# Optimization experiments

Hardware: AMD Instinct MI355X
Metric: run time of the kernel (lower is better)

The kernel has to match this reference:

```python
import jax, jax.numpy as jnp
import numpy as np


def setup_inputs() -> dict:
    key = jax.random.key(0)
    ks = jax.random.split(key, 6)
    B, T, I, H, O = 64, 512, 256, 512, 256
    stdv = 1.0 / np.sqrt(H)
    u = lambda k, shape: jax.random.uniform(k, shape, jnp.float32, -stdv, stdv)
    return {
        "x": jax.random.normal(ks[0], (B, T, I), jnp.float32),
        "W": u(ks[1], (I, 4 * H)),
        "U": u(ks[2], (H, 4 * H)),
        "bias": u(ks[3], (4 * H,)),
        "Wl": u(ks[4], (H, O)),
        "bl": u(ks[5], (O,)),
    }


def lstm_scan(x, W, U, bias):
    B, T, I = x.shape
    H = U.shape[0]
    # Precompute input projections for all timesteps in one big GEMM: [B,T,4H]
    x_proj = jnp.einsum("bti,ig->btg", x, W) + bias

    def step(carry, xp_t):
        h, c = carry
        gates = xp_t + h @ U  # [B, 4H]
        i_t = jax.nn.sigmoid(gates[:, :H])
        f_t = jax.nn.sigmoid(gates[:, H:2 * H])
        g_t = jnp.tanh(gates[:, 2 * H:3 * H])
        o_t = jax.nn.sigmoid(gates[:, 3 * H:])
        c_new = f_t * c + i_t * g_t
        h_new = o_t * jnp.tanh(c_new)
        return (h_new, c_new), h_new

    h0 = jnp.zeros((B, H), x.dtype)
    c0 = jnp.zeros((B, H), x.dtype)
    (h_T, c_T), hs = jax.lax.scan(step, (h0, c0), jnp.swapaxes(x_proj, 0, 1))
    hidden_seq = jnp.swapaxes(hs, 0, 1)  # [B, T, H]
    return hidden_seq, h_T, c_T


def reference(x, W, U, bias, Wl, bl):
    hidden_seq, h_T, c_T = lstm_scan(x, W, U, bias)
    out = hidden_seq @ Wl + bl  # [B, T, O]
    return out, (h_T, c_T)
```

## Files before the change

kernel.cpp:

```cpp
#include <hip/hip_runtime.h>
#include <stdint.h>

typedef uint16_t u16;
typedef uint32_t u32;
typedef unsigned long long u64;
typedef __attribute__((ext_vector_type(8))) __bf16 bf16x8;
typedef __attribute__((ext_vector_type(8))) short short8;
typedef __attribute__((ext_vector_type(4))) float floatx4;

__device__ __forceinline__ float bf2f(u16 u) {
  union { u32 i; float f; } v; v.i = ((u32)u) << 16; return v.f;
}
__device__ __forceinline__ u16 f2bf(float f) {
  union { float f; u32 i; } v; v.f = f;
  u32 i = v.i;
  return (u16)((i + 0x7FFFu + ((i >> 16) & 1u)) >> 16);
}
__device__ __forceinline__ float sigm(float x) { return 1.f / (1.f + __expf(-x)); }
__device__ __forceinline__ float tanh_f(float x) {
  x = fminf(15.f, fmaxf(-15.f, x));
  float e = __expf(2.f * x);
  return (e - 1.f) / (e + 1.f);
}

__global__ void transpose_f32_bf16(const float* __restrict__ src, u16* __restrict__ dst,
                                   int R, int C) {
  __shared__ u16 tile[32][33];
  int x = blockIdx.x * 32 + threadIdx.x;
#pragma unroll
  for (int j = 0; j < 4; ++j) {
    int y = blockIdx.y * 32 + threadIdx.y + j * 8;
    if (x < C && y < R) tile[threadIdx.y + j * 8][threadIdx.x] = f2bf(src[(size_t)y * C + x]);
  }
  __syncthreads();
  int x2 = blockIdx.y * 32 + threadIdx.x;
#pragma unroll
  for (int j = 0; j < 4; ++j) {
    int y2 = blockIdx.x * 32 + threadIdx.y + j * 8;
    if (x2 < R && y2 < C) dst[(size_t)y2 * R + x2] = tile[threadIdx.x][threadIdx.y + j * 8];
  }
}

__global__ __launch_bounds__(256) void gemm_a32_bt(
    const float* __restrict__ A, const u16* __restrict__ BT,
    const float* __restrict__ bias, u16* __restrict__ C,
    int M, int N, int K) {
  __shared__ __align__(16) u16 As[64 * 40];
  __shared__ __align__(16) u16 Bs[64 * 40];
  const int tid = threadIdx.x;
  const int wave = tid >> 6, lane = tid & 63;
  const int q4 = lane >> 4, n16 = lane & 15;
  const int mw = (wave >> 1) * 32, nw = (wave & 1) * 32;
  const int m0 = blockIdx.y * 64, n0 = blockIdx.x * 64;
  const int ldrow = tid >> 2, ldseg = (tid & 3) * 8;

  floatx4 acc[2][2] = {};
  for (int k0 = 0; k0 < K; k0 += 32) {
    const float* ap = A + (size_t)(m0 + ldrow) * K + k0 + ldseg;
    floatx4 a0 = *(const floatx4*)ap;
    floatx4 a1 = *(const floatx4*)(ap + 4);
    short8 s;
    s[0] = (short)f2bf(a0[0]); s[1] = (short)f2bf(a0[1]);
    s[2] = (short)f2bf(a0[2]); s[3] = (short)f2bf(a0[3]);
    s[4] = (short)f2bf(a1[0]); s[5] = (short)f2bf(a1[1]);
    s[6] = (short)f2bf(a1[2]); s[7] = (short)f2bf(a1[3]);
    *(short8*)(As + ldrow * 40 + ldseg) = s;
    *(short8*)(Bs + ldrow * 40 + ldseg) =
        *(const short8*)(BT + (size_t)(n0 + ldrow) * K + k0 + ldseg);
    __syncthreads();
#pragma unroll
    for (int mi = 0; mi < 2; ++mi) {
      bf16x8 a = *(const bf16x8*)(As + (mw + mi * 16 + n16) * 40 + q4 * 8);
#pragma unroll
      for (int ni = 0; ni < 2; ++ni) {
        bf16x8 b = *(const bf16x8*)(Bs + (nw + ni * 16 + n16) * 40 + q4 * 8);
        acc[mi][ni] = __builtin_amdgcn_mfma_f32_16x16x32_bf16(a, b, acc[mi][ni], 0, 0, 0);
      }
    }
    __syncthreads();
  }
#pragma unroll
  for (int mi = 0; mi < 2; ++mi)
#pragma unroll
    for (int ni = 0; ni < 2; ++ni) {
      int col = n0 + nw + ni * 16 + n16;
      float bv = bias[col];
#pragma unroll
      for (int r = 0; r < 4; ++r) {
        int m = m0 + mw + mi * 16 + q4 * 4 + r;
        C[(size_t)m * N + col] = f2bf(acc[mi][ni][r] + bv);
      }
    }
}

__global__ __launch_bounds__(256) void gemm_bt_f32out_perm(
    const u16* __restrict__ A, const u16* __restrict__ BT,
    const float* __restrict__ bias, float* __restrict__ C,
    int M, int N, int K) {
  __shared__ __align__(16) u16 As[64 * 40];
  __shared__ __align__(16) u16 Bs[64 * 40];
  const int tid = threadIdx.x;
  const int wave = tid >> 6, lane = tid & 63;
  const int q4 = lane >> 4, n16 = lane & 15;
  const int mw = (wave >> 1) * 32, nw = (wave & 1) * 32;
  const int m0 = blockIdx.y * 64, n0 = blockIdx.x * 64;
  const int ldrow = tid >> 2, ldseg = (tid & 3) * 8;

  const int mm = m0 + ldrow;
  const size_t slot = ((size_t)((mm >> 13) * 512 + ((mm & 8191) >> 4))) * 8192
                      + (mm & 15) * 16;

  floatx4 acc[2][2] = {};
  for (int k0 = 0; k0 < K; k0 += 32) {
    int kk = k0 + ldseg;
    *(short8*)(As + ldrow * 40 + ldseg) =
        *(const short8*)(A + slot + (kk >> 4) * 256 + (kk & 15));
    *(short8*)(Bs + ldrow * 40 + ldseg) =
        *(const short8*)(BT + (size_t)(n0 + ldrow) * K + k0 + ldseg);
    __syncthreads();
#pragma unroll
    for (int mi = 0; mi < 2; ++mi) {
      bf16x8 a = *(const bf16x8*)(As + (mw + mi * 16 + n16) * 40 + q4 * 8);
#pragma unroll
      for (int ni = 0; ni < 2; ++ni) {
        bf16x8 b = *(const bf16x8*)(Bs + (nw + ni * 16 + n16) * 40 + q4 * 8);
        acc[mi][ni] = __builtin_amdgcn_mfma_f32_16x16x32_bf16(a, b, acc[mi][ni], 0, 0, 0);
      }
    }
    __syncthreads();
  }
#pragma unroll
  for (int mi = 0; mi < 2; ++mi)
#pragma unroll
    for (int ni = 0; ni < 2; ++ni) {
      int col = n0 + nw + ni * 16 + n16;
      float bv = bias[col];
#pragma unroll
      for (int r = 0; r < 4; ++r) {
        int m = m0 + mw + mi * 16 + q4 * 4 + r;
        int orow = ((m >> 13) * 16 + (m & 15)) * 512 + ((m & 8191) >> 4);
        C[(size_t)orow * N + col] = acc[mi][ni][r] + bv;
      }
    }
}

#define T_STEPS 512
#define HLSZ (16 * 520)

#define LSTM_STEP(XC, XN, TT)                                                  \
  {                                                                            \
    const int t = (TT);                                                        \
    const int tn = (t + 1) & (T_STEPS - 1);                                    \
                   \
    _Pragma("unroll")                                                          \
    for (int qg = 0; qg < 4; ++qg)                                             \
      _Pragma("unroll")                                                        \
      for (int r = 0; r < 4; ++r)                                              \
        XN[qg * 4 + r] = xp_base[((size_t)(q4 * 4 + r) * T_STEPS + tn) * 2048  \
                                 + qg * 512 + cb + n];                         \
    __asm__ volatile("" ::: "memory");                                         \
    floatx4 acc[4] = {};                                                       \
    if (t > 0) {                                                               \
      const u64* hsrc = (const u64*)(hT_all)                                   \
                        + (size_t)(g * T_STEPS + (t - 1)) * 2048;              \
      u64 v[8];                                                                \
      for (;;) {                                                               \
        _Pragma("unroll")                                                      \
        for (int it = 0; it < 8; ++it)                                         \
          v[it] = __hip_atomic_load(hsrc + it * 256 + tid, __ATOMIC_RELAXED,   \
                                    __HIP_MEMORY_SCOPE_AGENT);                 \
        bool ok = true;                                                        \
        _Pragma("unroll")                                                      \
        for (int it = 0; it < 8; ++it) ok &= (v[it] != ~0ull);                 \
        if (ok) break;                                                         \
      }                                                                        \
      __asm__ volatile("" ::: "memory");                                       \
      u16* buf = hls + ((t - 1) & 1) * HLSZ;                                   \
      _Pragma("unroll")                                                        \
      for (int it = 0; it < 8; ++it) {                                         \
        int idx = it * 256 + tid;                                              \
        int tile = idx >> 6, w = idx & 63;                                     \
        *(u64*)(buf + (w >> 2) * 520 + tile * 16 + (w & 3) * 4) = v[it];       \
      }                                                                        \
      __syncthreads();                                                         \
      _Pragma("unroll")                                                        \
      for (int kt = 0; kt < 16; ++kt) {                                        \
        bf16x8 a = *(const bf16x8*)(buf + n * 520 + kt * 32 + q4 * 8);         \
        acc[0] = __builtin_amdgcn_mfma_f32_16x16x32_bf16(a, u[0][kt], acc[0], 0, 0, 0); \
        acc[1] = __builtin_amdgcn_mfma_f32_16x16x32_bf16(a, u[1][kt], acc[1], 0, 0, 0); \
        acc[2] = __builtin_amdgcn_mfma_f32_16x16x32_bf16(a, u[2][kt], acc[2], 0, 0, 0); \
        acc[3] = __builtin_amdgcn_mfma_f32_16x16x32_bf16(a, u[3][kt], acc[3], 0, 0, 0); \
      }                                                                        \
    }                                                                          \
    _Pragma("unroll")                                                          \
    for (int r = 0; r < 4; ++r) {                                              \
      float gi = sigm(acc[0][r] + bf2f(XC[r]));                                \
      float gf = sigm(acc[1][r] + bf2f(XC[4 + r]));                            \
      float gg = tanh_f(acc[2][r] + bf2f(XC[8 + r]));                          \
      float go = sigm(acc[3][r] + bf2f(XC[12 + r]));                           \
      float cn = gf * cst[r] + gi * gg;                                        \
      cst[r] = cn;                                                             \
      float hv = go * tanh_f(cn);                                              \
      int row = q4 * 4 + r;                                                    \
      hp[row * 16 + n] = f2bf(hv);                                             \
      if (t == T_STEPS - 1) {                                                  \
        out_hT[(g * 16 + row) * 512 + cb + n] = hv;                            \
        out_cT[(g * 16 + row) * 512 + cb + n] = cn;                            \
      }                                                                        \
    }                                                                          \
    __asm__ volatile("s_waitcnt lgkmcnt(0)" ::: "memory");                     \
    {                                                                          \
      u64 v = *(const u64*)(hp + (lane >> 2) * 16 + (lane & 3) * 4);           \
      u64* hdst = (u64*)(hT_all) + (size_t)(g * T_STEPS + t) * 2048            \
                  + p * 64 + lane;                                             \
      __hip_atomic_store(hdst, v, __ATOMIC_RELAXED, __HIP_MEMORY_SCOPE_AGENT); \
    }                                                                          \
  }

__global__ __launch_bounds__(256, 1) void lstm_scan(
    const u16* __restrict__ xp,
    const u16* __restrict__ UT,
    u16* __restrict__ hT_all,
    float* __restrict__ out_hT,
    float* __restrict__ out_cT) {
  const int bi = blockIdx.x;
  const int g = (bi & 7) >> 1;
  const int wgi = ((bi & 1) << 2) | (bi >> 3);
  const int tid = threadIdx.x;
  const int wave = tid >> 6;
  const int lane = tid & 63;
  const int n = lane & 15;
  const int q4 = lane >> 4;
  const int cb = wgi * 64 + wave * 16;
  const int p = wgi * 4 + wave;

  __shared__ __align__(16) u16 hls[2 * HLSZ];
  __shared__ __align__(8) u16 hstw[4 * 256];
  u16* hp = hstw + wave * 256;

  bf16x8 u[4][16];
#pragma unroll
  for (int qg = 0; qg < 4; ++qg) {
    const u16* up = UT + (size_t)(qg * 512 + cb + n) * 512;
#pragma unroll
    for (int kt = 0; kt < 16; ++kt)
      u[qg][kt] = *(const bf16x8*)(up + kt * 32 + q4 * 8);
  }

  float cst[4] = {0.f, 0.f, 0.f, 0.f};
  const u16* xp_base = xp + (size_t)(g * 16) * T_STEPS * 2048;

  u16 xa[16], xb[16];
#pragma unroll
  for (int qg = 0; qg < 4; ++qg)
#pragma unroll
    for (int r = 0; r < 4; ++r)
      xa[qg * 4 + r] = xp_base[((size_t)(q4 * 4 + r) * T_STEPS + 0) * 2048
                               + qg * 512 + cb + n];

#pragma unroll 1
  for (int t2 = 0; t2 < T_STEPS; t2 += 2) {
    LSTM_STEP(xa, xb, t2)
    LSTM_STEP(xb, xa, t2 + 1)
  }
}

extern "C" void kernel_launch(void* const* d_in, const int* in_sizes, int n_in,
                              void* d_out, int out_size, void* d_ws, size_t ws_size,
                              hipStream_t stream) {
  (void)in_sizes; (void)n_in; (void)out_size; (void)ws_size;
  const float* x    = (const float*)d_in[0];
  const float* W    = (const float*)d_in[1];
  const float* U    = (const float*)d_in[2];
  const float* bias = (const float*)d_in[3];
  const float* Wl   = (const float*)d_in[4];
  const float* bl   = (const float*)d_in[5];
  float* out = (float*)d_out;
  char* ws = (char*)d_ws;

  u16* xp     = (u16*)(ws + 0);
  u16* UT     = (u16*)(ws + 134217728);
  u16* WT     = (u16*)(ws + 136314880);
  u16* WlT    = (u16*)(ws + 137363456);
  u16* hT_all = (u16*)(ws + 137625600);

  hipMemsetAsync(hT_all, 0xFF, 33554432, stream);

  transpose_f32_bf16<<<dim3(2048 / 32, 256 / 32), dim3(32, 8), 0, stream>>>(W, WT, 256, 2048);
  transpose_f32_bf16<<<dim3(2048 / 32, 512 / 32), dim3(32, 8), 0, stream>>>(U, UT, 512, 2048);
  transpose_f32_bf16<<<dim3(256 / 32, 512 / 32), dim3(32, 8), 0, stream>>>(Wl, WlT, 512, 256);

  gemm_a32_bt<<<dim3(2048 / 64, 32768 / 64), 256, 0, stream>>>(x, WT, bias, xp, 32768, 2048, 256);

  lstm_scan<<<32, 256, 0, stream>>>(xp, UT, hT_all,
                                    out + 8388608, out + 8421376);

  gemm_bt_f32out_perm<<<dim3(256 / 64, 32768 / 64), 256, 0, stream>>>(
      hT_all, WlT, bl, out, 32768, 256, 512);
}
```

Measured before the change: 1.499 ms.

## Fuse input GEMM, LSTM scan and output GEMM into one persistent kernel with flag sync

```diff
diff --git a/kernel.cpp b/kernel.cpp
--- a/kernel.cpp
+++ b/kernel.cpp
@@ -41,116 +41,25 @@
   }
 }
 
-__global__ __launch_bounds__(256) void gemm_a32_bt(
-    const float* __restrict__ A, const u16* __restrict__ BT,
-    const float* __restrict__ bias, u16* __restrict__ C,
-    int M, int N, int K) {
-  __shared__ __align__(16) u16 As[64 * 40];
-  __shared__ __align__(16) u16 Bs[64 * 40];
-  const int tid = threadIdx.x;
-  const int wave = tid >> 6, lane = tid & 63;
-  const int q4 = lane >> 4, n16 = lane & 15;
-  const int mw = (wave >> 1) * 32, nw = (wave & 1) * 32;
-  const int m0 = blockIdx.y * 64, n0 = blockIdx.x * 64;
-  const int ldrow = tid >> 2, ldseg = (tid & 3) * 8;
-
-  floatx4 acc[2][2] = {};
-  for (int k0 = 0; k0 < K; k0 += 32) {
-    const float* ap = A + (size_t)(m0 + ldrow) * K + k0 + ldseg;
-    floatx4 a0 = *(const floatx4*)ap;
-    floatx4 a1 = *(const floatx4*)(ap + 4);
-    short8 s;
-    s[0] = (short)f2bf(a0[0]); s[1] = (short)f2bf(a0[1]);
-    s[2] = (short)f2bf(a0[2]); s[3] = (short)f2bf(a0[3]);
-    s[4] = (short)f2bf(a1[0]); s[5] = (short)f2bf(a1[1]);
-    s[6] = (short)f2bf(a1[2]); s[7] = (short)f2bf(a1[3]);
-    *(short8*)(As + ldrow * 40 + ldseg) = s;
-    *(short8*)(Bs + ldrow * 40 + ldseg) =
-        *(const short8*)(BT + (size_t)(n0 + ldrow) * K + k0 + ldseg);
-    __syncthreads();
-#pragma unroll
-    for (int mi = 0; mi < 2; ++mi) {
-      bf16x8 a = *(const bf16x8*)(As + (mw + mi * 16 + n16) * 40 + q4 * 8);
-#pragma unroll
-      for (int ni = 0; ni < 2; ++ni) {
-        bf16x8 b = *(const bf16x8*)(Bs + (nw + ni * 16 + n16) * 40 + q4 * 8);
-        acc[mi][ni] = __builtin_amdgcn_mfma_f32_16x16x32_bf16(a, b, acc[mi][ni], 0, 0, 0);
-      }
-    }
-    __syncthreads();
-  }
-#pragma unroll
-  for (int mi = 0; mi < 2; ++mi)
-#pragma unroll
-    for (int ni = 0; ni < 2; ++ni) {
-      int col = n0 + nw + ni * 16 + n16;
-      float bv = bias[col];
-#pragma unroll
-      for (int r = 0; r < 4; ++r) {
-        int m = m0 + mw + mi * 16 + q4 * 4 + r;
-        C[(size_t)m * N + col] = f2bf(acc[mi][ni][r] + bv);
-      }
-    }
-}
-
-__global__ __launch_bounds__(256) void gemm_bt_f32out_perm(
-    const u16* __restrict__ A, const u16* __restrict__ BT,
-    const float* __restrict__ bias, float* __restrict__ C,
-    int M, int N, int K) {
-  __shared__ __align__(16) u16 As[64 * 40];
-  __shared__ __align__(16) u16 Bs[64 * 40];
-  const int tid = threadIdx.x;
-  const int wave = tid >> 6, lane = tid & 63;
-  const int q4 = lane >> 4, n16 = lane & 15;
-  const int mw = (wave >> 1) * 32, nw = (wave & 1) * 32;
-  const int m0 = blockIdx.y * 64, n0 = blockIdx.x * 64;
-  const int ldrow = tid >> 2, ldseg = (tid & 3) * 8;
-
-  const int mm = m0 + ldrow;
-  const size_t slot = ((size_t)((mm >> 13) * 512 + ((mm & 8191) >> 4))) * 8192
-                      + (mm & 15) * 16;
-
-  floatx4 acc[2][2] = {};
-  for (int k0 = 0; k0 < K; k0 += 32) {
-    int kk = k0 + ldseg;
-    *(short8*)(As + ldrow * 40 + ldseg) =
-        *(const short8*)(A + slot + (kk >> 4) * 256 + (kk & 15));
-    *(short8*)(Bs + ldrow * 40 + ldseg) =
-        *(const short8*)(BT + (size_t)(n0 + ldrow) * K + k0 + ldseg);
-    __syncthreads();
-#pragma unroll
-    for (int mi = 0; mi < 2; ++mi) {
-      bf16x8 a = *(const bf16x8*)(As + (mw + mi * 16 + n16) * 40 + q4 * 8);
-#pragma unroll
-      for (int ni = 0; ni < 2; ++ni) {
-        bf16x8 b = *(const bf16x8*)(Bs + (nw + ni * 16 + n16) * 40 + q4 * 8);
-        acc[mi][ni] = __builtin_amdgcn_mfma_f32_16x16x32_bf16(a, b, acc[mi][ni], 0, 0, 0);
-      }
-    }
-    __syncthreads();
-  }
-#pragma unroll
-  for (int mi = 0; mi < 2; ++mi)
-#pragma unroll
-    for (int ni = 0; ni < 2; ++ni) {
-      int col = n0 + nw + ni * 16 + n16;
-      float bv = bias[col];
-#pragma unroll
-      for (int r = 0; r < 4; ++r) {
-        int m = m0 + mw + mi * 16 + q4 * 4 + r;
-        int orow = ((m >> 13) * 16 + (m & 15)) * 512 + ((m & 8191) >> 4);
-        C[(size_t)orow * N + col] = acc[mi][ni][r] + bv;
-      }
-    }
-}
-
 #define T_STEPS 512
 #define HLSZ (16 * 520)
+#define NWORK 224
 
 #define LSTM_STEP(XC, XN, TT)                                                  \
   {                                                                            \
     const int t = (TT);                                                        \
     const int tn = (t + 1) & (T_STEPS - 1);                                    \
+          \
+    if (((tn) & 63) == 0 && t < T_STEPS - 1) {                                 \
+      _Pragma("unroll")                                                        \
+      for (int r = 0; r < 4; ++r) {                                            \
+        const u32* cc = ctr + ((g * 16 + q4 * 4 + r) * 8 + (tn >> 6));         \
+        while (__hip_atomic_load(cc, __ATOMIC_RELAXED,                         \
+                                 __HIP_MEMORY_SCOPE_AGENT) < 32u)              \
+          __builtin_amdgcn_s_sleep(2);                                         \
+      }                                                                        \
+      __asm__ volatile("" ::: "memory");                                       \
+    }                                                                          \
                    \
     _Pragma("unroll")                                                          \
     for (int qg = 0; qg < 4; ++qg)                                             \
@@ -217,25 +126,143 @@
     }                                                                          \
   }
 
-__global__ __launch_bounds__(256, 1) void lstm_scan(
-    const u16* __restrict__ xp,
+__global__ __launch_bounds__(256, 1) void fused_lstm(
+    const float* __restrict__ x,
+    const u16* __restrict__ WT,
+    const float* __restrict__ bias,
+    u16* __restrict__ xp,
     const u16* __restrict__ UT,
     u16* __restrict__ hT_all,
+    const u16* __restrict__ WlT,
+    const float* __restrict__ bl,
+    float* __restrict__ outC,
     float* __restrict__ out_hT,
-    float* __restrict__ out_cT) {
+    float* __restrict__ out_cT,
+    u32* __restrict__ ctr) {
+  __shared__ __align__(16) u16 smem[2 * HLSZ + 4 * 256];
   const int bi = blockIdx.x;
+  const int tid = threadIdx.x;
+
+  if (bi >= 32) {
+    u16* As = smem;
+    u16* Bs = smem + 64 * 40;
+    const int wid = bi - 32;
+    const int wave = tid >> 6, lane = tid & 63;
+    const int q4 = lane >> 4, n16 = lane & 15;
+    const int mw = (wave >> 1) * 32, nw = (wave & 1) * 32;
+    const int ldrow = tid >> 2, ldseg = (tid & 3) * 8;
+
+    for (int j = wid; j < 16384; j += NWORK) {
+      const int tch = j >> 11;
+      const int rem = j & 2047;
+      const int b = rem >> 5, nt = rem & 31;
+      const int m0 = b * 512 + tch * 64, n0 = nt * 64;
+      floatx4 acc[2][2] = {};
+      for (int k0 = 0; k0 < 256; k0 += 32) {
+        const float* ap = x + (size_t)(m0 + ldrow) * 256 + k0 + ldseg;
+        floatx4 a0 = *(const floatx4*)ap;
+        floatx4 a1 = *(const floatx4*)(ap + 4);
+        short8 s;
+        s[0] = (short)f2bf(a0[0]); s[1] = (short)f2bf(a0[1]);
+        s[2] = (short)f2bf(a0[2]); s[3] = (short)f2bf(a0[3]);
+        s[4] = (short)f2bf(a1[0]); s[5] = (short)f2bf(a1[1]);
+        s[6] = (short)f2bf(a1[2]); s[7] = (short)f2bf(a1[3]);
+        *(short8*)(As + ldrow * 40 + ldseg) = s;
+        *(short8*)(Bs + ldrow * 40 + ldseg) =
+            *(const short8*)(WT + (size_t)(n0 + ldrow) * 256 + k0 + ldseg);
+        __syncthreads();
+#pragma unroll
+        for (int mi = 0; mi < 2; ++mi) {
+          bf16x8 a = *(const bf16x8*)(As + (mw + mi * 16 + n16) * 40 + q4 * 8);
+#pragma unroll
+          for (int ni = 0; ni < 2; ++ni) {
+            bf16x8 bb = *(const bf16x8*)(Bs + (nw + ni * 16 + n16) * 40 + q4 * 8);
+            acc[mi][ni] = __builtin_amdgcn_mfma_f32_16x16x32_bf16(a, bb, acc[mi][ni], 0, 0, 0);
+          }
+        }
+        __syncthreads();
+      }
+#pragma unroll
+      for (int mi = 0; mi < 2; ++mi)
+#pragma unroll
+        for (int ni = 0; ni < 2; ++ni) {
+          int col = n0 + nw + ni * 16 + n16;
+          float bv = bias[col];
+#pragma unroll
+          for (int r = 0; r < 4; ++r) {
+            int m = m0 + mw + mi * 16 + q4 * 4 + r;
+            u16 val = f2bf(acc[mi][ni][r] + bv);
+            __hip_atomic_store(xp + (size_t)m * 2048 + col, val,
+                               __ATOMIC_RELAXED, __HIP_MEMORY_SCOPE_AGENT);
+          }
+        }
+      __asm__ volatile("s_waitcnt vmcnt(0)" ::: "memory");
+      __syncthreads();
+      if (tid == 0)
+        __hip_atomic_fetch_add(ctr + b * 8 + tch, 1u,
+                               __ATOMIC_RELAXED, __HIP_MEMORY_SCOPE_AGENT);
+    }
+
+    for (int j = wid; j < 2048; j += NWORK) {
+      const int tb = j >> 4, g2 = (j >> 2) & 3, nt = j & 3;
+      const int m0 = g2 * 8192 + tb * 64, n0 = nt * 64;
+      const int mm = m0 + ldrow;
+      const size_t slot = ((size_t)((mm >> 13) * 512 + ((mm & 8191) >> 4))) * 8192
+                          + (mm & 15) * 16;
+      floatx4 acc[2][2] = {};
+      for (int k0 = 0; k0 < 512; k0 += 32) {
+        int kk = k0 + ldseg;
+        const u64* ap64 = (const u64*)(hT_all + slot + (kk >> 4) * 256 + (kk & 15));
+        u64 lo, hi;
+        for (;;) {
+          lo = __hip_atomic_load(ap64, __ATOMIC_RELAXED, __HIP_MEMORY_SCOPE_AGENT);
+          hi = __hip_atomic_load(ap64 + 1, __ATOMIC_RELAXED, __HIP_MEMORY_SCOPE_AGENT);
+          if (lo != ~0ull && hi != ~0ull) break;
+          __builtin_amdgcn_s_sleep(8);
+        }
+        *(u64*)(As + ldrow * 40 + ldseg) = lo;
+        *(u64*)(As + ldrow * 40 + ldseg + 4) = hi;
+        *(short8*)(Bs + ldrow * 40 + ldseg) =
+            *(const short8*)(WlT + (size_t)(n0 + ldrow) * 512 + k0 + ldseg);
+        __syncthreads();
+#pragma unroll
+        for (int mi = 0; mi < 2; ++mi) {
+          bf16x8 a = *(const bf16x8*)(As + (mw + mi * 16 + n16) * 40 + q4 * 8);
+#pragma unroll
+          for (int ni = 0; ni < 2; ++ni) {
+            bf16x8 bb = *(const bf16x8*)(Bs + (nw + ni * 16 + n16) * 40 + q4 * 8);
+            acc[mi][ni] = __builtin_amdgcn_mfma_f32_16x16x32_bf16(a, bb, acc[mi][ni], 0, 0, 0);
+          }
+        }
+        __syncthreads();
+      }
+#pragma unroll
+      for (int mi = 0; mi < 2; ++mi)
+#pragma unroll
+        for (int ni = 0; ni < 2; ++ni) {
+          int col = n0 + nw + ni * 16 + n16;
+          float bv = bl[col];
+#pragma unroll
+          for (int r = 0; r < 4; ++r) {
+            int m = m0 + mw + mi * 16 + q4 * 4 + r;
+            int orow = ((m >> 13) * 16 + (m & 15)) * 512 + ((m & 8191) >> 4);
+            outC[(size_t)orow * 256 + col] = acc[mi][ni][r] + bv;
+          }
+        }
+    }
+    return;
+  }
+
+  u16* hls = smem;
+  u16* hstw = smem + 2 * HLSZ;
   const int g = (bi & 7) >> 1;
   const int wgi = ((bi & 1) << 2) | (bi >> 3);
-  const int tid = threadIdx.x;
   const int wave = tid >> 6;
   const int lane = tid & 63;
   const int n = lane & 15;
   const int q4 = lane >> 4;
   const int cb = wgi * 64 + wave * 16;
   const int p = wgi * 4 + wave;
-
-  __shared__ __align__(16) u16 hls[2 * HLSZ];
-  __shared__ __align__(8) u16 hstw[4 * 256];
   u16* hp = hstw + wave * 256;
 
   bf16x8 u[4][16];
@@ -249,6 +276,14 @@
 
   float cst[4] = {0.f, 0.f, 0.f, 0.f};
   const u16* xp_base = xp + (size_t)(g * 16) * T_STEPS * 2048;
+
+#pragma unroll
+  for (int r = 0; r < 4; ++r) {
+    const u32* cc = ctr + ((g * 16 + q4 * 4 + r) * 8 + 0);
+    while (__hip_atomic_load(cc, __ATOMIC_RELAXED, __HIP_MEMORY_SCOPE_AGENT) < 32u)
+      __builtin_amdgcn_s_sleep(2);
+  }
+  __asm__ volatile("" ::: "memory");
 
   u16 xa[16], xb[16];
 #pragma unroll
@@ -284,17 +319,15 @@
   u16* WlT    = (u16*)(ws + 137363456);
   u16* hT_all = (u16*)(ws + 137625600);
 
+  u32* ctr = (u32*)(out + 8388608);
+
   hipMemsetAsync(hT_all, 0xFF, 33554432, stream);
+  hipMemsetAsync(ctr, 0x00, 2048, stream);
 
   transpose_f32_bf16<<<dim3(2048 / 32, 256 / 32), dim3(32, 8), 0, stream>>>(W, WT, 256, 2048);
   transpose_f32_bf16<<<dim3(2048 / 32, 512 / 32), dim3(32, 8), 0, stream>>>(U, UT, 512, 2048);
   transpose_f32_bf16<<<dim3(256 / 32, 512 / 32), dim3(32, 8), 0, stream>>>(Wl, WlT, 512, 256);
 
-  gemm_a32_bt<<<dim3(2048 / 64, 32768 / 64), 256, 0, stream>>>(x, WT, bias, xp, 32768, 2048, 256);
-
-  lstm_scan<<<32, 256, 0, stream>>>(xp, UT, hT_all,
-                                    out + 8388608, out + 8421376);
-
-  gemm_bt_f32out_perm<<<dim3(256 / 64, 32768 / 64), 256, 0, stream>>>(
-      hT_all, WlT, bl, out, 32768, 256, 512);
-}
+  fused_lstm<<<256, 256, 0, stream>>>(x, WT, bias, xp, UT, hT_all, WlT, bl,
+                                      out, out + 8388608, out + 8421376, ctr);
+}
```

Result: faster. 1.441 ms (-3.9%).
